# Kernel optimization log

Hardware: AMD Instinct MI355X
Metric: run time of the kernel (lower is better)

The kernel has to match this reference:

```python
import math
import jax, jax.numpy as jnp
import numpy as np

B, S, D, H = 4, 1024, 1024, 16
HD = D // H
EPS = 1e-5


def _sinusoidal_encodings(length, d):
    pos = jnp.arange(length, dtype=jnp.float32)
    inv_freq = 1.0 / (10000.0 ** (jnp.arange(0.0, d, 2.0) / d))
    angles = pos[:, None] * inv_freq[None, :]  # [L, D/2]
    enc = jnp.zeros((length, d), dtype=jnp.float32)
    enc = enc.at[:, 0::2].set(jnp.sin(angles))
    enc = enc.at[:, 1::2].set(jnp.cos(angles))
    return enc


def _relative_shift(emb):
    # emb: [B, H, L, L] -- Transformer-XL shift trick
    b, h, l1, l2 = emb.shape
    padded = jnp.concatenate([jnp.zeros((b, h, l1, 1), emb.dtype), emb], axis=-1)
    padded = padded.reshape(b, h, l2 + 1, l1)
    return padded[:, :, 1:, :].reshape(b, h, l1, l2)


def setup_inputs() -> dict:
    key = jax.random.key(0)
    ks = jax.random.split(key, 12)
    s = 0.02
    inp = {
        "x": jax.random.normal(ks[0], (B, S, D), dtype=jnp.float32),
        "Wq": jax.random.normal(ks[1], (D, D), dtype=jnp.float32) * s,
        "bq": jnp.zeros((D,), jnp.float32),
        "Wk": jax.random.normal(ks[2], (D, D), dtype=jnp.float32) * s,
        "bk": jnp.zeros((D,), jnp.float32),
        "Wv": jax.random.normal(ks[3], (D, D), dtype=jnp.float32) * s,
        "bv": jnp.zeros((D,), jnp.float32),
        "Wpos": jax.random.normal(ks[4], (D, D), dtype=jnp.float32) * s,
        "Wf": jax.random.normal(ks[5], (D, D), dtype=jnp.float32) * s,
        "bf": jnp.zeros((D,), jnp.float32),
        "u": jax.random.normal(ks[6], (H, HD), dtype=jnp.float32) * s,
        "v": jax.random.normal(ks[7], (H, HD), dtype=jnp.float32) * s,
        "gamma": jnp.ones((D,), jnp.float32),
        "beta": jnp.zeros((D,), jnp.float32),
    }
    return inp


def reference(x, Wq, bq, Wk, bk, Wv, bv, Wpos, Wf, bf, u, v, gamma, beta):
    b, s, d = x.shape
    # LayerNorm
    mu = jnp.mean(x, axis=-1, keepdims=True)
    var = jnp.mean((x - mu) ** 2, axis=-1, keepdims=True)
    xn = (x - mu) * jax.lax.rsqrt(var + EPS) * gamma + beta

    pe = _sinusoidal_encodings(s, d)  # [S, D]

    q = (xn @ Wq + bq).reshape(b, s, H, HD)
    k = (xn @ Wk + bk).reshape(b, s, H, HD)
    val = (xn @ Wv + bv).reshape(b, s, H, HD)
    p = (pe @ Wpos).reshape(s, H, HD)

    # content-content and content-position scores
    AC = jnp.einsum("bihd,bjhd->bhij", q + u, k)
    BD = jnp.einsum("bihd,jhd->bhij", q + v, p)
    BD = _relative_shift(BD)

    attn = jax.nn.softmax((AC + BD) / math.sqrt(d), axis=-1)  # [B,H,S,S]
    out = jnp.einsum("bhij,bjhd->bihd", attn, val).reshape(b, s, d)
    out = out @ Wf + bf  # dropout is identity (p=0 / eval)
    return out
```

## Files before the change

kernel.cpp:

```cpp
#include <hip/hip_runtime.h>
#include <math.h>


typedef __bf16 bf16;
typedef __bf16 bf16x8 __attribute__((ext_vector_type(8)));
typedef __bf16 bf16x4 __attribute__((ext_vector_type(4)));
typedef float f32x4 __attribute__((ext_vector_type(4)));

#define S_ 1024
#define D_ 1024
#define PROWS 3136
#define POFF 1088

#define AS1 __attribute__((address_space(1)))
#define AS3 __attribute__((address_space(3)))

static __device__ __forceinline__ f32x4 mfma16(bf16x8 a, bf16x8 b, f32x4 c) {
  return __builtin_amdgcn_mfma_f32_16x16x32_bf16(a, b, c, 0, 0, 0);
}

static constexpr size_t OXN  = 0;
static constexpr size_t OWTQ = OXN  + (size_t)4096*1024*2;
static constexpr size_t OWTK = OWTQ + (size_t)1024*1024*2;
static constexpr size_t OWTV = OWTK + (size_t)1024*1024*2;
static constexpr size_t OWTP = OWTV + (size_t)1024*1024*2;
static constexpr size_t OWTF = OWTP + (size_t)1024*1024*2;
static constexpr size_t OPE  = OWTF + (size_t)1024*1024*2;
static constexpr size_t OQU  = OPE  + (size_t)1024*1024*2;
static constexpr size_t OQV  = OQU  + (size_t)64*1024*64*2;
static constexpr size_t OKB  = OQV  + (size_t)64*1024*64*2 + 256;
static constexpr size_t OVT  = OKB  + (size_t)64*1024*64*2;
static constexpr size_t OPP  = OVT  + (size_t)64*1024*64*2;
static constexpr size_t PPBYTES = (size_t)16*PROWS*64*2;
static constexpr size_t OOB  = OPP  + PPBYTES;
static constexpr size_t OBU  = OOB  + (size_t)4096*1024*2;
static constexpr size_t OBV2 = OBU  + 4096;

__global__ __launch_bounds__(256) void misc_kernel(
    const float* __restrict__ bq, const float* __restrict__ u,
    const float* __restrict__ v, float* __restrict__ bu, float* __restrict__ bv2,
    bf16* __restrict__ pe, uint4* __restrict__ pz) {
  int blk = blockIdx.x, t = threadIdx.x;
  if (blk < 1024) {
    int pos = blk;
    #pragma unroll
    for (int pp = 0; pp < 2; pp++) {
      int f = t + pp * 256;
      float inv = expf(-(2.0f * (float)f * (1.0f / 1024.0f)) * 9.210340371976184f);
      float ang = (float)pos * inv;
      pe[(size_t)pos * D_ + 2 * f]     = (bf16)sinf(ang);
      pe[(size_t)pos * D_ + 2 * f + 1] = (bf16)cosf(ang);
    }
  } else if (blk < 1024 + 1568) {
    int i = (blk - 1024) * 256 + t;
    pz[i] = make_uint4(0u, 0u, 0u, 0u);
  } else {
    int c = (blk - 2592) * 256 + t;
    if (c < 1024) { bu[c] = bq[c] + u[c]; bv2[c] = bq[c] + v[c]; }
  }
}

__global__ __launch_bounds__(256) void ln_kernel(
    const float* __restrict__ x, const float* __restrict__ gamma,
    const float* __restrict__ beta, bf16* __restrict__ xn) {
  int row = blockIdx.x;
  int t = threadIdx.x;
  const float4* xr = (const float4*)(x + (size_t)row * D_);
  float4 v = xr[t];
  float s  = v.x + v.y + v.z + v.w;
  float ss = v.x*v.x + v.y*v.y + v.z*v.z + v.w*v.w;
  for (int off = 32; off; off >>= 1) {
    s  += __shfl_xor(s, off);
    ss += __shfl_xor(ss, off);
  }
  __shared__ float red[8];
  int wid = t >> 6;
  if ((t & 63) == 0) { red[wid] = s; red[wid + 4] = ss; }
  __syncthreads();
  float S  = red[0] + red[1] + red[2] + red[3];
  float SS = red[4] + red[5] + red[6] + red[7];
  float mu = S * (1.f / 1024.f);
  float rstd = rsqrtf(SS * (1.f / 1024.f) - mu * mu + 1e-5f);
  float4 g  = ((const float4*)gamma)[t];
  float4 bb = ((const float4*)beta)[t];
  bf16x4 o;
  o[0] = (bf16)((v.x - mu) * rstd * g.x + bb.x);
  o[1] = (bf16)((v.y - mu) * rstd * g.y + bb.y);
  o[2] = (bf16)((v.z - mu) * rstd * g.z + bb.z);
  o[3] = (bf16)((v.w - mu) * rstd * g.w + bb.w);
  *(bf16x4*)(xn + (size_t)row * D_ + t * 4) = o;
}

__global__ __launch_bounds__(256) void wtrans5_kernel(
    const float* __restrict__ W0, const float* __restrict__ W1,
    const float* __restrict__ W2, const float* __restrict__ W3,
    const float* __restrict__ W4, bf16* __restrict__ outbase) {
  __shared__ float tile[32][33];
  int z = blockIdx.z;
  const float* W = z == 0 ? W0 : z == 1 ? W1 : z == 2 ? W2 : z == 3 ? W3 : W4;
  bf16* WT = outbase + (size_t)z * 1024 * 1024;
  int bx = blockIdx.x, by = blockIdx.y;
  int tx = threadIdx.x & 31, ty = threadIdx.x >> 5;
  #pragma unroll
  for (int i = 0; i < 4; i++)
    tile[ty + i * 8][tx] = W[(size_t)(by * 32 + ty + i * 8) * D_ + bx * 32 + tx];
  __syncthreads();
  #pragma unroll
  for (int i = 0; i < 4; i++)
    WT[(size_t)(bx * 32 + ty + i * 8) * D_ + by * 32 + tx] = (bf16)tile[tx][ty + i * 8];
}

__global__ __launch_bounds__(256) void gemm_qkv_kernel(
    const bf16* __restrict__ A, const bf16* __restrict__ BT,
    const float* __restrict__ bu, const float* __restrict__ bv2,
    const float* __restrict__ bk, const float* __restrict__ bv,
    bf16* __restrict__ quB, bf16* __restrict__ qvB,
    bf16* __restrict__ kbB, bf16* __restrict__ vtB) {
  __shared__ __align__(16) bf16 As[128 * 32];
  __shared__ __align__(16) bf16 Bs[128 * 32];
  int gx = gridDim.x;
  int lin = blockIdx.x + gx * blockIdx.y;
  int cpx = (gx * gridDim.y) >> 3;
  int swz = (lin & 7) * cpx + (lin >> 3);
  int bx = swz % gx, by = swz / gx;
  int m0 = by * 128, n0 = bx * 128;
  int sect = n0 >> 10;
  int t = threadIdx.x, l = t & 63, w = t >> 6;
  int lr = l & 15, lq = l >> 4;
  int wr = w >> 1, wc = w & 1;
  f32x4 acc[4][4];
  #pragma unroll
  for (int mi = 0; mi < 4; mi++)
    #pragma unroll
    for (int ni = 0; ni < 4; ni++) acc[mi][ni] = (f32x4){0.f, 0.f, 0.f, 0.f};
  int srow = l >> 2, scol = (l & 3) * 8;
  for (int kk = 0; kk < 1024; kk += 32) {
    #pragma unroll
    for (int c2 = 0; c2 < 2; c2++) {
      int ch = w * 2 + c2;
      const bf16* ga = A + (size_t)(m0 + ch * 16 + srow) * 1024 + kk + scol;
      __builtin_amdgcn_global_load_lds((const AS1 void*)ga, (AS3 void*)(As + ch * 512), 16, 0, 0);
      const bf16* gb = BT + (size_t)(n0 + ch * 16 + srow) * 1024 + kk + scol;
      __builtin_amdgcn_global_load_lds((const AS1 void*)gb, (AS3 void*)(Bs + ch * 512), 16, 0, 0);
    }
    __syncthreads();
    bf16x8 af[4], bfv[4];
    #pragma unroll
    for (int mi = 0; mi < 4; mi++)
      af[mi] = *(const bf16x8*)(As + (wr * 64 + mi * 16 + lr) * 32 + lq * 8);
    #pragma unroll
    for (int ni = 0; ni < 4; ni++)
      bfv[ni] = *(const bf16x8*)(Bs + (wc * 64 + ni * 16 + lr) * 32 + lq * 8);
    if (sect == 2) {
      #pragma unroll
      for (int mi = 0; mi < 4; mi++)
        #pragma unroll
        for (int ni = 0; ni < 4; ni++)
          acc[mi][ni] = mfma16(bfv[ni], af[mi], acc[mi][ni]);
    } else {
      #pragma unroll
      for (int mi = 0; mi < 4; mi++)
        #pragma unroll
        for (int ni = 0; ni < 4; ni++)
          acc[mi][ni] = mfma16(af[mi], bfv[ni], acc[mi][ni]);
    }
    __syncthreads();
  }
  if (sect == 2) {
    #pragma unroll
    for (int mi = 0; mi < 4; mi++)
      #pragma unroll
      for (int ni = 0; ni < 4; ni++)
        #pragma unroll
        for (int rr = 0; rr < 4; rr++) {
          int wcol = (n0 - 2048) + wc * 64 + ni * 16 + lq * 4 + rr;
          int srw  = m0 + wr * 64 + mi * 16 + lr;
          int b = srw >> 10, s = srw & 1023, h = wcol >> 6, hd = wcol & 63;
          vtB[(((size_t)(b * 16 + h)) * 64 + hd) * 1024 + s] =
              (bf16)(acc[mi][ni][rr] + bv[wcol]);
        }
  } else {
    #pragma unroll
    for (int mi = 0; mi < 4; mi++)
      #pragma unroll
      for (int ni = 0; ni < 4; ni++)
        #pragma unroll
        for (int rr = 0; rr < 4; rr++) {
          int row = m0 + wr * 64 + mi * 16 + lq * 4 + rr;
          int col = n0 + wc * 64 + ni * 16 + lr;
          float vv = acc[mi][ni][rr];
          int b = row >> 10, s = row & 1023;
          if (sect == 0) {
            int h = col >> 6, hd = col & 63;
            size_t idx = (((size_t)(b * 16 + h)) * 1024 + s) * 64 + hd;
            quB[idx] = (bf16)(vv + bu[col]);
            qvB[idx] = (bf16)(vv + bv2[col]);
          } else {
            int c = col - 1024, h = c >> 6, hd = c & 63;
            size_t idx = (((size_t)(b * 16 + h)) * 1024 + s) * 64 + hd;
            kbB[idx] = (bf16)(vv + bk[c]);
          }
        }
  }
}

template <int MODE>
__global__ __launch_bounds__(256) void gemm_kernel(
    const bf16* __restrict__ A, const bf16* __restrict__ BT,
    const float* __restrict__ bias0, void* __restrict__ out0) {
  __shared__ __align__(16) bf16 As[128 * 32];
  __shared__ __align__(16) bf16 Bs[128 * 32];
  int gx = gridDim.x;
  int lin = blockIdx.x + gx * blockIdx.y;
  int cpx = (gx * gridDim.y) >> 3;
  int swz = (lin & 7) * cpx + (lin >> 3);
  int bx = swz % gx, by = swz / gx;
  int m0 = by * 128, n0 = bx * 128;
  int t = threadIdx.x, l = t & 63, w = t >> 6;
  int lr = l & 15, lq = l >> 4;
  int wr = w >> 1, wc = w & 1;
  f32x4 acc[4][4];
  #pragma unroll
  for (int mi = 0; mi < 4; mi++)
    #pragma unroll
    for (int ni = 0; ni < 4; ni++) acc[mi][ni] = (f32x4){0.f, 0.f, 0.f, 0.f};
  int srow = l >> 2, scol = (l & 3) * 8;
  for (int kk = 0; kk < 1024; kk += 32) {
    #pragma unroll
    for (int c2 = 0; c2 < 2; c2++) {
      int ch = w * 2 + c2;
      const bf16* ga = A + (size_t)(m0 + ch * 16 + srow) * 1024 + kk + scol;
      __builtin_amdgcn_global_load_lds((const AS1 void*)ga, (AS3 void*)(As + ch * 512), 16, 0, 0);
      const bf16* gb = BT + (size_t)(n0 + ch * 16 + srow) * 1024 + kk + scol;
      __builtin_amdgcn_global_load_lds((const AS1 void*)gb, (AS3 void*)(Bs + ch * 512), 16, 0, 0);
    }
    __syncthreads();
    bf16x8 af[4], bfv[4];
    #pragma unroll
    for (int mi = 0; mi < 4; mi++)
      af[mi] = *(const bf16x8*)(As + (wr * 64 + mi * 16 + lr) * 32 + lq * 8);
    #pragma unroll
    for (int ni = 0; ni < 4; ni++)
      bfv[ni] = *(const bf16x8*)(Bs + (wc * 64 + ni * 16 + lr) * 32 + lq * 8);
    #pragma unroll
    for (int mi = 0; mi < 4; mi++)
      #pragma unroll
      for (int ni = 0; ni < 4; ni++)
        acc[mi][ni] = mfma16(af[mi], bfv[ni], acc[mi][ni]);
    __syncthreads();
  }
  #pragma unroll
  for (int mi = 0; mi < 4; mi++)
    #pragma unroll
    for (int ni = 0; ni < 4; ni++)
      #pragma unroll
      for (int rr = 0; rr < 4; rr++) {
        int row = m0 + wr * 64 + mi * 16 + lq * 4 + rr;
        int col = n0 + wc * 64 + ni * 16 + lr;
        float vv = acc[mi][ni][rr];
        if constexpr (MODE == 0) {
          ((float*)out0)[(size_t)row * 1024 + col] = vv + bias0[col];
        } else {
          int h = col >> 6, hd = col & 63;
          ((bf16*)out0)[((size_t)h * PROWS + POFF + row) * 64 + hd] = (bf16)vv;
        }
      }
}

__global__ __launch_bounds__(256) void attn_kernel(
    const bf16* __restrict__ qu, const bf16* __restrict__ qv,
    const bf16* __restrict__ kb, const bf16* __restrict__ vt,
    const bf16* __restrict__ ppad, bf16* __restrict__ ob) {
  int bid = blockIdx.x;
  int xcd = bid & 7, slot = bid >> 3;
  int g = slot >> 4, qblk = slot & 15;
  int bh = xcd + 8 * g;
  int h = bh & 15, b = bh >> 4;

  int t = threadIdx.x, l = t & 63, wid = t >> 6;
  int lr = l & 15, lq = l >> 4;
  int w0 = qblk * 64 + wid * 16;
  const bf16* quB = qu + (size_t)bh * S_ * 64;
  const bf16* qvB = qv + (size_t)bh * S_ * 64;
  const char* kBy = (const char*)(kb + (size_t)bh * S_ * 64);
  const char* vBy = (const char*)(vt + (size_t)bh * 64 * S_);
  const bf16* pH  = ppad + (size_t)h * PROWS * 64;

  __shared__ __align__(16) bf16 Kbuf[2][4096];
  __shared__ __align__(16) bf16 Vbuf[2][4096];
  __shared__ __align__(16) bf16 G1s[4][16][84];
  __shared__ __align__(16) bf16 G2s[4][16][84];
  bf16* PlW = &G1s[wid][0][0];

  bf16x8 aqu[2], aqv1[2], aqv2[2];
  #pragma unroll
  for (int ks = 0; ks < 2; ks++) {
    aqu[ks]  = *(const bf16x8*)(quB + (size_t)(w0 + lr) * 64 + ks * 32 + lq * 8);
    aqv1[ks] = *(const bf16x8*)(qvB + (size_t)(w0 + lr) * 64 + ks * 32 + lq * 8);
    aqv2[ks] = *(const bf16x8*)(qvB + (size_t)(w0 + 1 + lr) * 64 + ks * 32 + lq * 8);
  }
  bf16x8 ones;
  #pragma unroll
  for (int e = 0; e < 8; e++) ones[e] = (bf16)1.0f;

  float m_run[4];
  f32x4 accL = (f32x4){0.f, 0.f, 0.f, 0.f};
  f32x4 accO[4];
  #pragma unroll
  for (int rr = 0; rr < 4; rr++) m_run[rr] = -1e30f;
  #pragma unroll
  for (int nf = 0; nf < 4; nf++) accO[nf] = (f32x4){0.f, 0.f, 0.f, 0.f};

  const float SC = 0.045084220f;

  int srow8 = l >> 3;
  int scolb = (l & 7) * 16;
  auto stage = [&](int nb, int j0n) {
    #pragma unroll
    for (int ci = 0; ci < 4; ci++) {
      int c = wid * 4 + ci;
      int cc = c & 7;
      int row = cc * 8 + srow8;
      int colsrc = scolb ^ ((row & 7) << 4);
      if (c < 8) {
        const char* src = kBy + (size_t)(j0n + row) * 128 + colsrc;
        __builtin_amdgcn_global_load_lds((const AS1 void*)src,
            (AS3 void*)(&Kbuf[nb][cc * 512]), 16, 0, 0);
      } else {
        const char* src = vBy + (size_t)row * 2048 + j0n * 2 + colsrc;
        __builtin_amdgcn_global_load_lds((const AS1 void*)src,
            (AS3 void*)(&Vbuf[nb][cc * 512]), 16, 0, 0);
      }
    }
  };

  stage(0, 0);
  __syncthreads();

  for (int tt = 0; tt < 16; tt++) {
    int j0 = tt * 64;
    int cur = tt & 1;
    if (tt < 15) stage(cur ^ 1, j0 + 64);

    const char* Ks = (const char*)&Kbuf[cur][0];
    const char* Vs = (const char*)&Vbuf[cur][0];
    int d = w0 - j0;

    f32x4 accS[4];
    __builtin_amdgcn_s_setprio(1);
    #pragma unroll
    for (int nf = 0; nf < 4; nf++) {
      accS[nf] = (f32x4){0.f, 0.f, 0.f, 0.f};
      int rowk = nf * 16 + lr;
      #pragma unroll
      for (int ks = 0; ks < 2; ks++) {
        int off = ((rowk << 7) + (ks << 6) + (lq << 4)) ^ ((rowk & 7) << 4);
        bf16x8 bk8 = *(const bf16x8*)(Ks + off);
        accS[nf] = mfma16(aqu[ks], bk8, accS[nf]);
      }
    }
    __builtin_amdgcn_s_setprio(0);

    if (d >= 63) {
      int pb = 1023 - w0 + j0 - 15 + POFF;
      bf16x8 bp[10];
      #pragma unroll
      for (int gf = 0; gf < 5; gf++)
        #pragma unroll
        for (int ks = 0; ks < 2; ks++)
          bp[gf * 2 + ks] = *(const bf16x8*)(pH + (size_t)(pb + gf * 16 + lr) * 64 + ks * 32 + lq * 8);
      #pragma unroll
      for (int gf = 0; gf < 5; gf++) {
        f32x4 gg = (f32x4){0.f, 0.f, 0.f, 0.f};
        gg = mfma16(aqv1[0], bp[gf * 2 + 0], gg);
        gg = mfma16(aqv1[1], bp[gf * 2 + 1], gg);
        #pragma unroll
        for (int rr = 0; rr < 4; rr++) G1s[wid][lq * 4 + rr][gf * 16 + lr] = (bf16)gg[rr];
      }
    } else if (d <= -17) {
      int pb = j0 - w0 - 17 + POFF;
      bf16x8 bp[10];
      #pragma unroll
      for (int gf = 0; gf < 5; gf++)
        #pragma unroll
        for (int ks = 0; ks < 2; ks++)
          bp[gf * 2 + ks] = *(const bf16x8*)(pH + (size_t)(pb + gf * 16 + lr) * 64 + ks * 32 + lq * 8);
      #pragma unroll
      for (int gf = 0; gf < 5; gf++) {
        f32x4 gg = (f32x4){0.f, 0.f, 0.f, 0.f};
        gg = mfma16(aqv2[0], bp[gf * 2 + 0], gg);
        gg = mfma16(aqv2[1], bp[gf * 2 + 1], gg);
        #pragma unroll
        for (int rr = 0; rr < 4; rr++) G2s[wid][lq * 4 + rr][gf * 16 + lr] = (bf16)gg[rr];
      }
    } else {
      {
        int pb = 1023 - w0 + j0 - 15 + POFF;
        int gmax = (d + 15) >> 4; if (gmax > 4) gmax = 4;
        for (int gf = 0; gf <= gmax; gf++) {
          f32x4 gg = (f32x4){0.f, 0.f, 0.f, 0.f};
          #pragma unroll
          for (int ks = 0; ks < 2; ks++) {
            bf16x8 bp = *(const bf16x8*)(pH + (size_t)(pb + gf * 16 + lr) * 64 + ks * 32 + lq * 8);
            gg = mfma16(aqv1[ks], bp, gg);
          }
          #pragma unroll
          for (int rr = 0; rr < 4; rr++) G1s[wid][lq * 4 + rr][gf * 16 + lr] = (bf16)gg[rr];
        }
      }
      {
        int pb = j0 - w0 - 17 + POFF;
        int t2 = d + 17;
        int gmin = t2 > 0 ? (t2 >> 4) : 0;
        for (int gf = gmin; gf < 5; gf++) {
          f32x4 gg = (f32x4){0.f, 0.f, 0.f, 0.f};
          #pragma unroll
          for (int ks = 0; ks < 2; ks++) {
            bf16x8 bp = *(const bf16x8*)(pH + (size_t)(pb + gf * 16 + lr) * 64 + ks * 32 + lq * 8);
            gg = mfma16(aqv2[ks], bp, gg);
          }
          #pragma unroll
          for (int rr = 0; rr < 4; rr++) G2s[wid][lq * 4 + rr][gf * 16 + lr] = (bf16)gg[rr];
        }
      }
    }

    float sc[4][4];
    if (d >= 63) {
      #pragma unroll
      for (int nf = 0; nf < 4; nf++)
        #pragma unroll
        for (int rr = 0; rr < 4; rr++) {
          int ii = lq * 4 + rr;
          int u = nf * 16 + lr - ii + 15;
          sc[nf][rr] = (accS[nf][rr] + (float)G1s[wid][ii][u]) * SC;
        }
    } else if (d <= -17) {
      #pragma unroll
      for (int nf = 0; nf < 4; nf++)
        #pragma unroll
        for (int rr = 0; rr < 4; rr++) {
          int ii = lq * 4 + rr;
          int u = nf * 16 + lr - ii + 15;
          sc[nf][rr] = (accS[nf][rr] + (float)G2s[wid][ii][u]) * SC;
        }
    } else {
      #pragma unroll
      for (int nf = 0; nf < 4; nf++)
        #pragma unroll
        for (int rr = 0; rr < 4; rr++) {
          int ii = lq * 4 + rr;
          int jj = nf * 16 + lr;
          int dd = jj - ii;
          int u = dd + 15;
          float g1v = (float)G1s[wid][ii][u];
          float g2v = (float)G2s[wid][ii][u];
          float bd = dd <= d ? g1v : (dd == d + 1 ? 0.f : g2v);
          sc[nf][rr] = (accS[nf][rr] + bd) * SC;
        }
    }

    float lmax[4];
    #pragma unroll
    for (int rr = 0; rr < 4; rr++)
      lmax[rr] = fmaxf(fmaxf(sc[0][rr], sc[1][rr]), fmaxf(sc[2][rr], sc[3][rr]));
    bool ok = (lmax[0] <= m_run[0] + 8.f) && (lmax[1] <= m_run[1] + 8.f) &&
              (lmax[2] <= m_run[2] + 8.f) && (lmax[3] <= m_run[3] + 8.f);
    if (!__all((int)ok)) {
      float rmax[4];
      #pragma unroll
      for (int rr = 0; rr < 4; rr++) rmax[rr] = lmax[rr];
      #pragma unroll
      for (int st = 1; st < 16; st <<= 1)
        #pragma unroll
        for (int rr = 0; rr < 4; rr++) rmax[rr] = fmaxf(rmax[rr], __shfl_xor(rmax[rr], st));
      #pragma unroll
      for (int rr = 0; rr < 4; rr++) {
        float mnew = fmaxf(m_run[rr], rmax[rr]);
        float sv = exp2f(m_run[rr] - mnew);
        m_run[rr] = mnew;
        accL[rr] *= sv;
        #pragma unroll
        for (int nf = 0; nf < 4; nf++) accO[nf][rr] *= sv;
      }
    }

    #pragma unroll
    for (int nf = 0; nf < 4; nf++)
      #pragma unroll
      for (int rr = 0; rr < 4; rr++) {
        float p = exp2f(sc[nf][rr] - m_run[rr]);
        PlW[(lq * 4 + rr) * 72 + nf * 16 + lr] = (bf16)p;
      }

    bf16x8 ap[2];
    #pragma unroll
    for (int ks = 0; ks < 2; ks++)
      ap[ks] = *(const bf16x8*)(PlW + lr * 72 + ks * 32 + lq * 8);
    __builtin_amdgcn_s_setprio(1);
    #pragma unroll
    for (int ks = 0; ks < 2; ks++) accL = mfma16(ap[ks], ones, accL);
    #pragma unroll
    for (int nf = 0; nf < 4; nf++) {
      int rowd = nf * 16 + lr;
      #pragma unroll
      for (int ks = 0; ks < 2; ks++) {
        int off = ((rowd << 7) + (ks << 6) + (lq << 4)) ^ ((rowd & 7) << 4);
        bf16x8 bv8 = *(const bf16x8*)(Vs + off);
        accO[nf] = mfma16(ap[ks], bv8, accO[nf]);
      }
    }
    __builtin_amdgcn_s_setprio(0);

    __syncthreads();
  }

  #pragma unroll
  for (int nf = 0; nf < 4; nf++)
    #pragma unroll
    for (int rr = 0; rr < 4; rr++) {
      int i = w0 + lq * 4 + rr;
      float o = accO[nf][rr] / accL[rr];
      ob[((size_t)(b * S_ + i)) * 1024 + h * 64 + nf * 16 + lr] = (bf16)o;
    }
}

extern "C" void kernel_launch(void* const* d_in, const int* in_sizes, int n_in,
                              void* d_out, int out_size, void* d_ws, size_t ws_size,
                              hipStream_t stream) {
  const float* x     = (const float*)d_in[0];
  const float* Wq    = (const float*)d_in[1];
  const float* bq    = (const float*)d_in[2];
  const float* Wk    = (const float*)d_in[3];
  const float* bk    = (const float*)d_in[4];
  const float* Wv    = (const float*)d_in[5];
  const float* bv    = (const float*)d_in[6];
  const float* Wpos  = (const float*)d_in[7];
  const float* Wf    = (const float*)d_in[8];
  const float* bf_   = (const float*)d_in[9];
  const float* u     = (const float*)d_in[10];
  const float* v     = (const float*)d_in[11];
  const float* gamma = (const float*)d_in[12];
  const float* beta  = (const float*)d_in[13];

  char* ws = (char*)d_ws;
  bf16* xn  = (bf16*)(ws + OXN);
  bf16* wtq = (bf16*)(ws + OWTQ);
  bf16* wtp = (bf16*)(ws + OWTP);
  bf16* wtf = (bf16*)(ws + OWTF);
  bf16* pe  = (bf16*)(ws + OPE);
  bf16* quB = (bf16*)(ws + OQU);
  bf16* qvB = (bf16*)(ws + OQV);
  bf16* kbB = (bf16*)(ws + OKB);
  bf16* vtB = (bf16*)(ws + OVT);
  bf16* ppd = (bf16*)(ws + OPP);
  bf16* obB = (bf16*)(ws + OOB);
  float* bu  = (float*)(ws + OBU);
  float* bv2 = (float*)(ws + OBV2);

  misc_kernel<<<2596, 256, 0, stream>>>(bq, u, v, bu, bv2, pe, (uint4*)(ws + OPP));
  ln_kernel<<<4096, 256, 0, stream>>>(x, gamma, beta, xn);
  wtrans5_kernel<<<dim3(32, 32, 5), 256, 0, stream>>>(Wq, Wk, Wv, Wpos, Wf, wtq);

  gemm_qkv_kernel<<<dim3(24, 32), 256, 0, stream>>>(xn, wtq, bu, bv2, bk, bv,
                                                    quB, qvB, kbB, vtB);
  gemm_kernel<3><<<dim3(8, 8), 256, 0, stream>>>(pe, wtp, nullptr, ppd);

  attn_kernel<<<1024, 256, 0, stream>>>(quB, qvB, kbB, vtB, ppd, obB);

  gemm_kernel<0><<<dim3(8, 32), 256, 0, stream>>>(obB, wtf, bf_, (float*)d_out);
}
```

Before: 263.8 us.

## Double attention block to 8 waves and transpose relative-position scratch layout

The attention kernel now runs 512 threads (8 waves) per block covering 128 query rows, with half as many blocks. Each K/V tile staged into shared memory is therefore shared by twice as many waves, and each wave issues half the staging loads. The per-wave position-score scratch is stored transposed with a stride of 18 so the MFMA results can be written as paired bf16 stores and read back with fewer bank conflicts. The cost is larger blocks, more shared memory per block and possibly lower occupancy or worse tail balance.

```diff
diff --git a/kernel.cpp b/kernel.cpp
--- a/kernel.cpp
+++ b/kernel.cpp
@@ -5,6 +5,7 @@
 typedef __bf16 bf16;
 typedef __bf16 bf16x8 __attribute__((ext_vector_type(8)));
 typedef __bf16 bf16x4 __attribute__((ext_vector_type(4)));
+typedef __bf16 bf16x2 __attribute__((ext_vector_type(2)));
 typedef float f32x4 __attribute__((ext_vector_type(4)));
 
 #define S_ 1024
@@ -267,19 +268,19 @@
       }
 }
 
-__global__ __launch_bounds__(256) void attn_kernel(
+__global__ __launch_bounds__(512) void attn_kernel(
     const bf16* __restrict__ qu, const bf16* __restrict__ qv,
     const bf16* __restrict__ kb, const bf16* __restrict__ vt,
     const bf16* __restrict__ ppad, bf16* __restrict__ ob) {
   int bid = blockIdx.x;
   int xcd = bid & 7, slot = bid >> 3;
-  int g = slot >> 4, qblk = slot & 15;
+  int g = slot >> 3, qblk = slot & 7;
   int bh = xcd + 8 * g;
   int h = bh & 15, b = bh >> 4;
 
   int t = threadIdx.x, l = t & 63, wid = t >> 6;
   int lr = l & 15, lq = l >> 4;
-  int w0 = qblk * 64 + wid * 16;
+  int w0 = qblk * 128 + wid * 16;
   const bf16* quB = qu + (size_t)bh * S_ * 64;
   const bf16* qvB = qv + (size_t)bh * S_ * 64;
   const char* kBy = (const char*)(kb + (size_t)bh * S_ * 64);
@@ -288,9 +289,11 @@
 
   __shared__ __align__(16) bf16 Kbuf[2][4096];
   __shared__ __align__(16) bf16 Vbuf[2][4096];
-  __shared__ __align__(16) bf16 G1s[4][16][84];
-  __shared__ __align__(16) bf16 G2s[4][16][84];
-  bf16* PlW = &G1s[wid][0][0];
+  __shared__ __align__(16) bf16 Gt1[8][1440];
+  __shared__ __align__(16) bf16 Gt2[8][1440];
+  bf16* G1w = &Gt1[wid][0];
+  bf16* G2w = &Gt2[wid][0];
+  bf16* PlW = G1w;
 
   bf16x8 aqu[2], aqv1[2], aqv2[2];
   #pragma unroll
@@ -317,8 +320,8 @@
   int scolb = (l & 7) * 16;
   auto stage = [&](int nb, int j0n) {
     #pragma unroll
-    for (int ci = 0; ci < 4; ci++) {
-      int c = wid * 4 + ci;
+    for (int ci = 0; ci < 2; ci++) {
+      int c = wid * 2 + ci;
       int cc = c & 7;
       int row = cc * 8 + srow8;
       int colsrc = scolb ^ ((row & 7) << 4);
@@ -374,8 +377,12 @@
         f32x4 gg = (f32x4){0.f, 0.f, 0.f, 0.f};
         gg = mfma16(aqv1[0], bp[gf * 2 + 0], gg);
         gg = mfma16(aqv1[1], bp[gf * 2 + 1], gg);
-        #pragma unroll
-        for (int rr = 0; rr < 4; rr++) G1s[wid][lq * 4 + rr][gf * 16 + lr] = (bf16)gg[rr];
+        bf16x2 p0, p1;
+        p0[0] = (bf16)gg[0]; p0[1] = (bf16)gg[1];
+        p1[0] = (bf16)gg[2]; p1[1] = (bf16)gg[3];
+        int base = (gf * 16 + lr) * 18 + lq * 4;
+        *(bf16x2*)(&G1w[base])     = p0;
+        *(bf16x2*)(&G1w[base + 2]) = p1;
       }
     } else if (d <= -17) {
       int pb = j0 - w0 - 17 + POFF;
@@ -390,8 +397,12 @@
         f32x4 gg = (f32x4){0.f, 0.f, 0.f, 0.f};
         gg = mfma16(aqv2[0], bp[gf * 2 + 0], gg);
         gg = mfma16(aqv2[1], bp[gf * 2 + 1], gg);
-        #pragma unroll
-        for (int rr = 0; rr < 4; rr++) G2s[wid][lq * 4 + rr][gf * 16 + lr] = (bf16)gg[rr];
+        bf16x2 p0, p1;
+        p0[0] = (bf16)gg[0]; p0[1] = (bf16)gg[1];
+        p1[0] = (bf16)gg[2]; p1[1] = (bf16)gg[3];
+        int base = (gf * 16 + lr) * 18 + lq * 4;
+        *(bf16x2*)(&G2w[base])     = p0;
+        *(bf16x2*)(&G2w[base + 2]) = p1;
       }
     } else {
       {
@@ -404,8 +415,12 @@
             bf16x8 bp = *(const bf16x8*)(pH + (size_t)(pb + gf * 16 + lr) * 64 + ks * 32 + lq * 8);
             gg = mfma16(aqv1[ks], bp, gg);
           }
-          #pragma unroll
-          for (int rr = 0; rr < 4; rr++) G1s[wid][lq * 4 + rr][gf * 16 + lr] = (bf16)gg[rr];
+          bf16x2 p0, p1;
+          p0[0] = (bf16)gg[0]; p0[1] = (bf16)gg[1];
+          p1[0] = (bf16)gg[2]; p1[1] = (bf16)gg[3];
+          int base = (gf * 16 + lr) * 18 + lq * 4;
+          *(bf16x2*)(&G1w[base])     = p0;
+          *(bf16x2*)(&G1w[base + 2]) = p1;
         }
       }
       {
@@ -419,8 +434,12 @@
             bf16x8 bp = *(const bf16x8*)(pH + (size_t)(pb + gf * 16 + lr) * 64 + ks * 32 + lq * 8);
             gg = mfma16(aqv2[ks], bp, gg);
           }
-          #pragma unroll
-          for (int rr = 0; rr < 4; rr++) G2s[wid][lq * 4 + rr][gf * 16 + lr] = (bf16)gg[rr];
+          bf16x2 p0, p1;
+          p0[0] = (bf16)gg[0]; p0[1] = (bf16)gg[1];
+          p1[0] = (bf16)gg[2]; p1[1] = (bf16)gg[3];
+          int base = (gf * 16 + lr) * 18 + lq * 4;
+          *(bf16x2*)(&G2w[base])     = p0;
+          *(bf16x2*)(&G2w[base + 2]) = p1;
         }
       }
     }
@@ -433,7 +452,7 @@
         for (int rr = 0; rr < 4; rr++) {
           int ii = lq * 4 + rr;
           int u = nf * 16 + lr - ii + 15;
-          sc[nf][rr] = (accS[nf][rr] + (float)G1s[wid][ii][u]) * SC;
+          sc[nf][rr] = (accS[nf][rr] + (float)G1w[u * 18 + ii]) * SC;
         }
     } else if (d <= -17) {
       #pragma unroll
@@ -442,7 +461,7 @@
         for (int rr = 0; rr < 4; rr++) {
           int ii = lq * 4 + rr;
           int u = nf * 16 + lr - ii + 15;
-          sc[nf][rr] = (accS[nf][rr] + (float)G2s[wid][ii][u]) * SC;
+          sc[nf][rr] = (accS[nf][rr] + (float)G2w[u * 18 + ii]) * SC;
         }
     } else {
       #pragma unroll
@@ -453,8 +472,8 @@
           int jj = nf * 16 + lr;
           int dd = jj - ii;
           int u = dd + 15;
-          float g1v = (float)G1s[wid][ii][u];
-          float g2v = (float)G2s[wid][ii][u];
+          float g1v = (float)G1w[u * 18 + ii];
+          float g2v = (float)G2w[u * 18 + ii];
           float bd = dd <= d ? g1v : (dd == d + 1 ? 0.f : g2v);
           sc[nf][rr] = (accS[nf][rr] + bd) * SC;
         }
@@ -566,7 +585,7 @@
                                                     quB, qvB, kbB, vtB);
   gemm_kernel<3><<<dim3(8, 8), 256, 0, stream>>>(pe, wtp, nullptr, ppd);
 
-  attn_kernel<<<1024, 256, 0, stream>>>(quB, qvB, kbB, vtB, ppd, obB);
+  attn_kernel<<<512, 512, 0, stream>>>(quB, qvB, kbB, vtB, ppd, obB);
 
   gemm_kernel<0><<<dim3(8, 32), 256, 0, stream>>>(obB, wtf, bf_, (float*)d_out);
 }
```

Result: slower. 279.9 us (+6.1%).

## Load K and V fragments directly from global memory instead of LDS double-buffer

Applied to the files above, without the earlier changes.

Removes the shared-memory double-buffered staging of K and V tiles (global_load_lds) and the per-iteration block barrier. Each wave now reads its K and V MFMA fragments straight from global memory into registers. This drops the LDS traffic and synchronisation but makes each of the 4 waves fetch the same K/V tile separately, relying on cache reuse, and leaves no prefetch to hide load latency.

```diff
diff --git a/kernel.cpp b/kernel.cpp
--- a/kernel.cpp
+++ b/kernel.cpp
@@ -282,12 +282,10 @@
   int w0 = qblk * 64 + wid * 16;
   const bf16* quB = qu + (size_t)bh * S_ * 64;
   const bf16* qvB = qv + (size_t)bh * S_ * 64;
-  const char* kBy = (const char*)(kb + (size_t)bh * S_ * 64);
-  const char* vBy = (const char*)(vt + (size_t)bh * 64 * S_);
+  const bf16* kB  = kb + (size_t)bh * S_ * 64;
+  const bf16* vtB = vt + (size_t)bh * 64 * S_;
   const bf16* pH  = ppad + (size_t)h * PROWS * 64;
 
-  __shared__ __align__(16) bf16 Kbuf[2][4096];
-  __shared__ __align__(16) bf16 Vbuf[2][4096];
   __shared__ __align__(16) bf16 G1s[4][16][84];
   __shared__ __align__(16) bf16 G2s[4][16][84];
   bf16* PlW = &G1s[wid][0][0];
@@ -313,51 +311,23 @@
 
   const float SC = 0.045084220f;
 
-  int srow8 = l >> 3;
-  int scolb = (l & 7) * 16;
-  auto stage = [&](int nb, int j0n) {
-    #pragma unroll
-    for (int ci = 0; ci < 4; ci++) {
-      int c = wid * 4 + ci;
-      int cc = c & 7;
-      int row = cc * 8 + srow8;
-      int colsrc = scolb ^ ((row & 7) << 4);
-      if (c < 8) {
-        const char* src = kBy + (size_t)(j0n + row) * 128 + colsrc;
-        __builtin_amdgcn_global_load_lds((const AS1 void*)src,
-            (AS3 void*)(&Kbuf[nb][cc * 512]), 16, 0, 0);
-      } else {
-        const char* src = vBy + (size_t)row * 2048 + j0n * 2 + colsrc;
-        __builtin_amdgcn_global_load_lds((const AS1 void*)src,
-            (AS3 void*)(&Vbuf[nb][cc * 512]), 16, 0, 0);
-      }
-    }
-  };
-
-  stage(0, 0);
-  __syncthreads();
-
   for (int tt = 0; tt < 16; tt++) {
     int j0 = tt * 64;
-    int cur = tt & 1;
-    if (tt < 15) stage(cur ^ 1, j0 + 64);
-
-    const char* Ks = (const char*)&Kbuf[cur][0];
-    const char* Vs = (const char*)&Vbuf[cur][0];
     int d = w0 - j0;
 
     f32x4 accS[4];
+    bf16x8 kfr[8];
+    #pragma unroll
+    for (int nf = 0; nf < 4; nf++)
+      #pragma unroll
+      for (int ks = 0; ks < 2; ks++)
+        kfr[nf * 2 + ks] = *(const bf16x8*)(kB + (size_t)(j0 + nf * 16 + lr) * 64 + ks * 32 + lq * 8);
     __builtin_amdgcn_s_setprio(1);
     #pragma unroll
     for (int nf = 0; nf < 4; nf++) {
       accS[nf] = (f32x4){0.f, 0.f, 0.f, 0.f};
-      int rowk = nf * 16 + lr;
-      #pragma unroll
-      for (int ks = 0; ks < 2; ks++) {
-        int off = ((rowk << 7) + (ks << 6) + (lq << 4)) ^ ((rowk & 7) << 4);
-        bf16x8 bk8 = *(const bf16x8*)(Ks + off);
-        accS[nf] = mfma16(aqu[ks], bk8, accS[nf]);
-      }
+      accS[nf] = mfma16(aqu[0], kfr[nf * 2 + 0], accS[nf]);
+      accS[nf] = mfma16(aqu[1], kfr[nf * 2 + 1], accS[nf]);
     }
     __builtin_amdgcn_s_setprio(0);
 
@@ -497,22 +467,21 @@
     #pragma unroll
     for (int ks = 0; ks < 2; ks++)
       ap[ks] = *(const bf16x8*)(PlW + lr * 72 + ks * 32 + lq * 8);
+    bf16x8 vfr[8];
+    #pragma unroll
+    for (int nf = 0; nf < 4; nf++)
+      #pragma unroll
+      for (int ks = 0; ks < 2; ks++)
+        vfr[nf * 2 + ks] = *(const bf16x8*)(vtB + (size_t)(nf * 16 + lr) * 1024 + j0 + ks * 32 + lq * 8);
     __builtin_amdgcn_s_setprio(1);
     #pragma unroll
     for (int ks = 0; ks < 2; ks++) accL = mfma16(ap[ks], ones, accL);
     #pragma unroll
     for (int nf = 0; nf < 4; nf++) {
-      int rowd = nf * 16 + lr;
-      #pragma unroll
-      for (int ks = 0; ks < 2; ks++) {
-        int off = ((rowd << 7) + (ks << 6) + (lq << 4)) ^ ((rowd & 7) << 4);
-        bf16x8 bv8 = *(const bf16x8*)(Vs + off);
-        accO[nf] = mfma16(ap[ks], bv8, accO[nf]);
-      }
+      accO[nf] = mfma16(ap[0], vfr[nf * 2 + 0], accO[nf]);
+      accO[nf] = mfma16(ap[1], vfr[nf * 2 + 1], accO[nf]);
     }
     __builtin_amdgcn_s_setprio(0);
-
-    __syncthreads();
   }
 
   #pragma unroll
```

After: 340.8 us. +29.2%, slower.

## Merge prep kernels, fuse position GEMM into QKV GEMM, double-buffer LDS

Applied to the files above, without the earlier changes.

Merges the layernorm, weight-transpose and misc setup kernels into one prep launch, and folds the positional projection GEMM into the QKV GEMM grid as extra blocks. Both GEMM kernels now double-buffer LDS tiles so the next K slice is prefetched while the current one is computed. The aim is fewer launches, fuller GPU occupancy for the small pos GEMM, and hidden global-load latency. In exchange LDS use doubles and prep blocks mix code paths. Double buffering with a single barrier per iteration risks a race on the buffer being overwritten.

```diff
diff --git a/kernel.cpp b/kernel.cpp
--- a/kernel.cpp
+++ b/kernel.cpp
@@ -36,95 +36,105 @@
 static constexpr size_t OBU  = OOB  + (size_t)4096*1024*2;
 static constexpr size_t OBV2 = OBU  + 4096;
 
-__global__ __launch_bounds__(256) void misc_kernel(
+__global__ __launch_bounds__(256) void prep_kernel(
+    const float* __restrict__ x, const float* __restrict__ gamma,
+    const float* __restrict__ beta, bf16* __restrict__ xn,
+    const float* __restrict__ W0, const float* __restrict__ W1,
+    const float* __restrict__ W2, const float* __restrict__ W3,
+    const float* __restrict__ W4, bf16* __restrict__ outbase,
     const float* __restrict__ bq, const float* __restrict__ u,
     const float* __restrict__ v, float* __restrict__ bu, float* __restrict__ bv2,
     bf16* __restrict__ pe, uint4* __restrict__ pz) {
   int blk = blockIdx.x, t = threadIdx.x;
-  if (blk < 1024) {
-    int pos = blk;
-    #pragma unroll
-    for (int pp = 0; pp < 2; pp++) {
-      int f = t + pp * 256;
-      float inv = expf(-(2.0f * (float)f * (1.0f / 1024.0f)) * 9.210340371976184f);
-      float ang = (float)pos * inv;
-      pe[(size_t)pos * D_ + 2 * f]     = (bf16)sinf(ang);
-      pe[(size_t)pos * D_ + 2 * f + 1] = (bf16)cosf(ang);
-    }
-  } else if (blk < 1024 + 1568) {
-    int i = (blk - 1024) * 256 + t;
-    pz[i] = make_uint4(0u, 0u, 0u, 0u);
+  __shared__ float tile[32][33];
+  __shared__ float red[8];
+  if (blk < 4096) {
+    int row = blk;
+    const float4* xr = (const float4*)(x + (size_t)row * D_);
+    float4 vv = xr[t];
+    float s  = vv.x + vv.y + vv.z + vv.w;
+    float ss = vv.x*vv.x + vv.y*vv.y + vv.z*vv.z + vv.w*vv.w;
+    for (int off = 32; off; off >>= 1) {
+      s  += __shfl_xor(s, off);
+      ss += __shfl_xor(ss, off);
+    }
+    int wid = t >> 6;
+    if ((t & 63) == 0) { red[wid] = s; red[wid + 4] = ss; }
+    __syncthreads();
+    float S  = red[0] + red[1] + red[2] + red[3];
+    float SS = red[4] + red[5] + red[6] + red[7];
+    float mu = S * (1.f / 1024.f);
+    float rstd = rsqrtf(SS * (1.f / 1024.f) - mu * mu + 1e-5f);
+    float4 g  = ((const float4*)gamma)[t];
+    float4 bb = ((const float4*)beta)[t];
+    bf16x4 o;
+    o[0] = (bf16)((vv.x - mu) * rstd * g.x + bb.x);
+    o[1] = (bf16)((vv.y - mu) * rstd * g.y + bb.y);
+    o[2] = (bf16)((vv.z - mu) * rstd * g.z + bb.z);
+    o[3] = (bf16)((vv.w - mu) * rstd * g.w + bb.w);
+    *(bf16x4*)(xn + (size_t)row * D_ + t * 4) = o;
+  } else if (blk < 9216) {
+    int idx = blk - 4096;
+    int z = idx >> 10, rem = idx & 1023;
+    int bx = rem & 31, by = rem >> 5;
+    const float* W = z == 0 ? W0 : z == 1 ? W1 : z == 2 ? W2 : z == 3 ? W3 : W4;
+    bf16* WT = outbase + (size_t)z * 1024 * 1024;
+    int tx = t & 31, ty = t >> 5;
+    #pragma unroll
+    for (int i = 0; i < 4; i++)
+      tile[ty + i * 8][tx] = W[(size_t)(by * 32 + ty + i * 8) * D_ + bx * 32 + tx];
+    __syncthreads();
+    #pragma unroll
+    for (int i = 0; i < 4; i++)
+      WT[(size_t)(bx * 32 + ty + i * 8) * D_ + by * 32 + tx] = (bf16)tile[tx][ty + i * 8];
   } else {
-    int c = (blk - 2592) * 256 + t;
-    if (c < 1024) { bu[c] = bq[c] + u[c]; bv2[c] = bq[c] + v[c]; }
+    int mblk = blk - 9216;
+    if (mblk < 1024) {
+      int pos = mblk;
+      #pragma unroll
+      for (int pp = 0; pp < 2; pp++) {
+        int f = t + pp * 256;
+        float inv = expf(-(2.0f * (float)f * (1.0f / 1024.0f)) * 9.210340371976184f);
+        float ang = (float)pos * inv;
+        pe[(size_t)pos * D_ + 2 * f]     = (bf16)sinf(ang);
+        pe[(size_t)pos * D_ + 2 * f + 1] = (bf16)cosf(ang);
+      }
+    } else if (mblk < 1024 + 1568) {
+      int i = (mblk - 1024) * 256 + t;
+      pz[i] = make_uint4(0u, 0u, 0u, 0u);
+    } else {
+      int c = (mblk - 2592) * 256 + t;
+      if (c < 1024) { bu[c] = bq[c] + u[c]; bv2[c] = bq[c] + v[c]; }
+    }
   }
 }
 
-__global__ __launch_bounds__(256) void ln_kernel(
-    const float* __restrict__ x, const float* __restrict__ gamma,
-    const float* __restrict__ beta, bf16* __restrict__ xn) {
-  int row = blockIdx.x;
-  int t = threadIdx.x;
-  const float4* xr = (const float4*)(x + (size_t)row * D_);
-  float4 v = xr[t];
-  float s  = v.x + v.y + v.z + v.w;
-  float ss = v.x*v.x + v.y*v.y + v.z*v.z + v.w*v.w;
-  for (int off = 32; off; off >>= 1) {
-    s  += __shfl_xor(s, off);
-    ss += __shfl_xor(ss, off);
-  }
-  __shared__ float red[8];
-  int wid = t >> 6;
-  if ((t & 63) == 0) { red[wid] = s; red[wid + 4] = ss; }
-  __syncthreads();
-  float S  = red[0] + red[1] + red[2] + red[3];
-  float SS = red[4] + red[5] + red[6] + red[7];
-  float mu = S * (1.f / 1024.f);
-  float rstd = rsqrtf(SS * (1.f / 1024.f) - mu * mu + 1e-5f);
-  float4 g  = ((const float4*)gamma)[t];
-  float4 bb = ((const float4*)beta)[t];
-  bf16x4 o;
-  o[0] = (bf16)((v.x - mu) * rstd * g.x + bb.x);
-  o[1] = (bf16)((v.y - mu) * rstd * g.y + bb.y);
-  o[2] = (bf16)((v.z - mu) * rstd * g.z + bb.z);
-  o[3] = (bf16)((v.w - mu) * rstd * g.w + bb.w);
-  *(bf16x4*)(xn + (size_t)row * D_ + t * 4) = o;
-}
-
-__global__ __launch_bounds__(256) void wtrans5_kernel(
-    const float* __restrict__ W0, const float* __restrict__ W1,
-    const float* __restrict__ W2, const float* __restrict__ W3,
-    const float* __restrict__ W4, bf16* __restrict__ outbase) {
-  __shared__ float tile[32][33];
-  int z = blockIdx.z;
-  const float* W = z == 0 ? W0 : z == 1 ? W1 : z == 2 ? W2 : z == 3 ? W3 : W4;
-  bf16* WT = outbase + (size_t)z * 1024 * 1024;
-  int bx = blockIdx.x, by = blockIdx.y;
-  int tx = threadIdx.x & 31, ty = threadIdx.x >> 5;
-  #pragma unroll
-  for (int i = 0; i < 4; i++)
-    tile[ty + i * 8][tx] = W[(size_t)(by * 32 + ty + i * 8) * D_ + bx * 32 + tx];
-  __syncthreads();
-  #pragma unroll
-  for (int i = 0; i < 4; i++)
-    WT[(size_t)(bx * 32 + ty + i * 8) * D_ + by * 32 + tx] = (bf16)tile[tx][ty + i * 8];
-}
-
-__global__ __launch_bounds__(256) void gemm_qkv_kernel(
-    const bf16* __restrict__ A, const bf16* __restrict__ BT,
+__global__ __launch_bounds__(256) void gemm_qkvp_kernel(
+    const bf16* __restrict__ xn, const bf16* __restrict__ pe,
+    const bf16* __restrict__ BT,
     const float* __restrict__ bu, const float* __restrict__ bv2,
     const float* __restrict__ bk, const float* __restrict__ bv,
     bf16* __restrict__ quB, bf16* __restrict__ qvB,
-    bf16* __restrict__ kbB, bf16* __restrict__ vtB) {
-  __shared__ __align__(16) bf16 As[128 * 32];
-  __shared__ __align__(16) bf16 Bs[128 * 32];
-  int gx = gridDim.x;
-  int lin = blockIdx.x + gx * blockIdx.y;
-  int cpx = (gx * gridDim.y) >> 3;
-  int swz = (lin & 7) * cpx + (lin >> 3);
-  int bx = swz % gx, by = swz / gx;
-  int m0 = by * 128, n0 = bx * 128;
-  int sect = n0 >> 10;
+    bf16* __restrict__ kbB, bf16* __restrict__ vtB, bf16* __restrict__ ppd) {
+  __shared__ __align__(16) bf16 As[2][4096];
+  __shared__ __align__(16) bf16 Bs[2][4096];
+  int lin = blockIdx.x;
+  int swz = (lin & 7) * 104 + (lin >> 3);
+  int m0, n0, sect;
+  const bf16* Abase;
+  int nrow0;
+  if (swz < 768) {
+    int bx = swz % 24, by = swz / 24;
+    m0 = by * 128; n0 = bx * 128;
+    sect = n0 >> 10;
+    Abase = xn; nrow0 = n0;
+  } else {
+    int pp = swz - 768;
+    int bx = pp & 7, by = pp >> 3;
+    m0 = by * 128; n0 = bx * 128;
+    sect = 3;
+    Abase = pe; nrow0 = 3072 + n0;
+  }
   int t = threadIdx.x, l = t & 63, w = t >> 6;
   int lr = l & 15, lq = l >> 4;
   int wr = w >> 1, wc = w & 1;
@@ -134,23 +144,28 @@
     #pragma unroll
     for (int ni = 0; ni < 4; ni++) acc[mi][ni] = (f32x4){0.f, 0.f, 0.f, 0.f};
   int srow = l >> 2, scol = (l & 3) * 8;
-  for (int kk = 0; kk < 1024; kk += 32) {
+  auto stage = [&](int nb, int kk) {
     #pragma unroll
     for (int c2 = 0; c2 < 2; c2++) {
       int ch = w * 2 + c2;
-      const bf16* ga = A + (size_t)(m0 + ch * 16 + srow) * 1024 + kk + scol;
-      __builtin_amdgcn_global_load_lds((const AS1 void*)ga, (AS3 void*)(As + ch * 512), 16, 0, 0);
-      const bf16* gb = BT + (size_t)(n0 + ch * 16 + srow) * 1024 + kk + scol;
-      __builtin_amdgcn_global_load_lds((const AS1 void*)gb, (AS3 void*)(Bs + ch * 512), 16, 0, 0);
-    }
-    __syncthreads();
+      const bf16* ga = Abase + (size_t)(m0 + ch * 16 + srow) * 1024 + kk + scol;
+      __builtin_amdgcn_global_load_lds((const AS1 void*)ga, (AS3 void*)(&As[nb][ch * 512]), 16, 0, 0);
+      const bf16* gb = BT + (size_t)(nrow0 + ch * 16 + srow) * 1024 + kk + scol;
+      __builtin_amdgcn_global_load_lds((const AS1 void*)gb, (AS3 void*)(&Bs[nb][ch * 512]), 16, 0, 0);
+    }
+  };
+  stage(0, 0);
+  __syncthreads();
+  for (int it = 0; it < 32; it++) {
+    int cur = it & 1;
+    if (it < 31) stage(cur ^ 1, (it + 1) * 32);
     bf16x8 af[4], bfv[4];
     #pragma unroll
     for (int mi = 0; mi < 4; mi++)
-      af[mi] = *(const bf16x8*)(As + (wr * 64 + mi * 16 + lr) * 32 + lq * 8);
+      af[mi] = *(const bf16x8*)(&As[cur][(wr * 64 + mi * 16 + lr) * 32 + lq * 8]);
     #pragma unroll
     for (int ni = 0; ni < 4; ni++)
-      bfv[ni] = *(const bf16x8*)(Bs + (wc * 64 + ni * 16 + lr) * 32 + lq * 8);
+      bfv[ni] = *(const bf16x8*)(&Bs[cur][(wc * 64 + ni * 16 + lr) * 32 + lq * 8]);
     if (sect == 2) {
       #pragma unroll
       for (int mi = 0; mi < 4; mi++)
@@ -178,6 +193,18 @@
           int b = srw >> 10, s = srw & 1023, h = wcol >> 6, hd = wcol & 63;
           vtB[(((size_t)(b * 16 + h)) * 64 + hd) * 1024 + s] =
               (bf16)(acc[mi][ni][rr] + bv[wcol]);
+        }
+  } else if (sect == 3) {
+    #pragma unroll
+    for (int mi = 0; mi < 4; mi++)
+      #pragma unroll
+      for (int ni = 0; ni < 4; ni++)
+        #pragma unroll
+        for (int rr = 0; rr < 4; rr++) {
+          int row = m0 + wr * 64 + mi * 16 + lq * 4 + rr;
+          int col = n0 + wc * 64 + ni * 16 + lr;
+          int h = col >> 6, hd = col & 63;
+          ppd[((size_t)h * PROWS + POFF + row) * 64 + hd] = (bf16)acc[mi][ni][rr];
         }
   } else {
     #pragma unroll
@@ -204,12 +231,11 @@
   }
 }
 
-template <int MODE>
-__global__ __launch_bounds__(256) void gemm_kernel(
+__global__ __launch_bounds__(256) void gemm_final_kernel(
     const bf16* __restrict__ A, const bf16* __restrict__ BT,
-    const float* __restrict__ bias0, void* __restrict__ out0) {
-  __shared__ __align__(16) bf16 As[128 * 32];
-  __shared__ __align__(16) bf16 Bs[128 * 32];
+    const float* __restrict__ bias0, float* __restrict__ out0) {
+  __shared__ __align__(16) bf16 As[2][4096];
+  __shared__ __align__(16) bf16 Bs[2][4096];
   int gx = gridDim.x;
   int lin = blockIdx.x + gx * blockIdx.y;
   int cpx = (gx * gridDim.y) >> 3;
@@ -225,23 +251,28 @@
     #pragma unroll
     for (int ni = 0; ni < 4; ni++) acc[mi][ni] = (f32x4){0.f, 0.f, 0.f, 0.f};
   int srow = l >> 2, scol = (l & 3) * 8;
-  for (int kk = 0; kk < 1024; kk += 32) {
+  auto stage = [&](int nb, int kk) {
     #pragma unroll
     for (int c2 = 0; c2 < 2; c2++) {
       int ch = w * 2 + c2;
       const bf16* ga = A + (size_t)(m0 + ch * 16 + srow) * 1024 + kk + scol;
-      __builtin_amdgcn_global_load_lds((const AS1 void*)ga, (AS3 void*)(As + ch * 512), 16, 0, 0);
+      __builtin_amdgcn_global_load_lds((const AS1 void*)ga, (AS3 void*)(&As[nb][ch * 512]), 16, 0, 0);
       const bf16* gb = BT + (size_t)(n0 + ch * 16 + srow) * 1024 + kk + scol;
-      __builtin_amdgcn_global_load_lds((const AS1 void*)gb, (AS3 void*)(Bs + ch * 512), 16, 0, 0);
-    }
-    __syncthreads();
+      __builtin_amdgcn_global_load_lds((const AS1 void*)gb, (AS3 void*)(&Bs[nb][ch * 512]), 16, 0, 0);
+    }
+  };
+  stage(0, 0);
+  __syncthreads();
+  for (int it = 0; it < 32; it++) {
+    int cur = it & 1;
+    if (it < 31) stage(cur ^ 1, (it + 1) * 32);
     bf16x8 af[4], bfv[4];
     #pragma unroll
     for (int mi = 0; mi < 4; mi++)
-      af[mi] = *(const bf16x8*)(As + (wr * 64 + mi * 16 + lr) * 32 + lq * 8);
+      af[mi] = *(const bf16x8*)(&As[cur][(wr * 64 + mi * 16 + lr) * 32 + lq * 8]);
     #pragma unroll
     for (int ni = 0; ni < 4; ni++)
-      bfv[ni] = *(const bf16x8*)(Bs + (wc * 64 + ni * 16 + lr) * 32 + lq * 8);
+      bfv[ni] = *(const bf16x8*)(&Bs[cur][(wc * 64 + ni * 16 + lr) * 32 + lq * 8]);
     #pragma unroll
     for (int mi = 0; mi < 4; mi++)
       #pragma unroll
@@ -257,13 +288,7 @@
       for (int rr = 0; rr < 4; rr++) {
         int row = m0 + wr * 64 + mi * 16 + lq * 4 + rr;
         int col = n0 + wc * 64 + ni * 16 + lr;
-        float vv = acc[mi][ni][rr];
-        if constexpr (MODE == 0) {
-          ((float*)out0)[(size_t)row * 1024 + col] = vv + bias0[col];
-        } else {
-          int h = col >> 6, hd = col & 63;
-          ((bf16*)out0)[((size_t)h * PROWS + POFF + row) * 64 + hd] = (bf16)vv;
-        }
+        out0[(size_t)row * 1024 + col] = acc[mi][ni][rr] + bias0[col];
       }
 }
 
@@ -546,7 +571,6 @@
   char* ws = (char*)d_ws;
   bf16* xn  = (bf16*)(ws + OXN);
   bf16* wtq = (bf16*)(ws + OWTQ);
-  bf16* wtp = (bf16*)(ws + OWTP);
   bf16* wtf = (bf16*)(ws + OWTF);
   bf16* pe  = (bf16*)(ws + OPE);
   bf16* quB = (bf16*)(ws + OQU);
@@ -558,15 +582,14 @@
   float* bu  = (float*)(ws + OBU);
   float* bv2 = (float*)(ws + OBV2);
 
-  misc_kernel<<<2596, 256, 0, stream>>>(bq, u, v, bu, bv2, pe, (uint4*)(ws + OPP));
-  ln_kernel<<<4096, 256, 0, stream>>>(x, gamma, beta, xn);
-  wtrans5_kernel<<<dim3(32, 32, 5), 256, 0, stream>>>(Wq, Wk, Wv, Wpos, Wf, wtq);
-
-  gemm_qkv_kernel<<<dim3(24, 32), 256, 0, stream>>>(xn, wtq, bu, bv2, bk, bv,
-                                                    quB, qvB, kbB, vtB);
-  gemm_kernel<3><<<dim3(8, 8), 256, 0, stream>>>(pe, wtp, nullptr, ppd);
+  prep_kernel<<<11812, 256, 0, stream>>>(x, gamma, beta, xn,
+                                         Wq, Wk, Wv, Wpos, Wf, wtq,
+                                         bq, u, v, bu, bv2, pe, (uint4*)(ws + OPP));
+
+  gemm_qkvp_kernel<<<832, 256, 0, stream>>>(xn, pe, wtq, bu, bv2, bk, bv,
+                                            quB, qvB, kbB, vtB, ppd);
 
   attn_kernel<<<1024, 256, 0, stream>>>(quB, qvB, kbB, vtB, ppd, obB);
 
-  gemm_kernel<0><<<dim3(8, 32), 256, 0, stream>>>(obB, wtf, bf_, (float*)d_out);
+  gemm_final_kernel<<<dim3(8, 32), 256, 0, stream>>>(obB, wtf, bf_, (float*)d_out);
 }
```

Result: slower. 270.8 us (+2.7%).
